# Kernel optimization log

Measured on AMD Instinct MI355X. Metric: run time of the kernel, lower is better.

Reference implementation:

```python
import jax, jax.numpy as jnp
import numpy as np

SEQ_LEN = 79
D_MODEL = 1024
BATCH = 512


def setup_inputs() -> dict:
    key = jax.random.key(0)
    ks = jax.random.split(key, 6)
    d = D_MODEL
    inp = {
        "x": jax.random.normal(ks[0], (BATCH, SEQ_LEN, d), dtype=jnp.float32),
        "piece_w": jax.random.normal(ks[1], (d, 6), dtype=jnp.float32) / np.sqrt(d),
        "piece_b": jnp.zeros((6,), dtype=jnp.float32),
        "color_w": jax.random.normal(ks[2], (d, 1), dtype=jnp.float32) / np.sqrt(d),
        "color_b": jnp.zeros((1,), dtype=jnp.float32),
        "mlp1_w": jax.random.normal(ks[3], (15, 32), dtype=jnp.float32) / np.sqrt(15.0),
        "mlp1_b": jnp.zeros((32,), dtype=jnp.float32),
        "mlp2_w": jax.random.normal(ks[4], (32, 8), dtype=jnp.float32) / np.sqrt(32.0),
        "mlp2_b": jnp.zeros((8,), dtype=jnp.float32),
    }
    return inp


def _spatial_feats(n, dtype):
    # dx, dy between board squares (idx < 64), zeros for non-board tokens
    idx = jnp.arange(n)
    is_board = idx < 64
    xc = jnp.where(is_board, idx // 8, 0)
    yc = jnp.where(is_board, idx % 8, 0)
    dx = xc[:, None] - xc[None, :]
    dy = yc[:, None] - yc[None, :]
    return jnp.stack([dx, dy], axis=-1).astype(dtype)  # (N, N, 2)


def reference(x, piece_w, piece_b, color_w, color_b, mlp1_w, mlp1_b, mlp2_w, mlp2_b):
    B, N, d = x.shape
    spatial = _spatial_feats(N, x.dtype)                      # (N, N, 2)
    piece_emb = jnp.einsum("bnd,de->bne", x, piece_w) + piece_b   # (B, N, 6)
    color_emb = jnp.einsum("bnd,de->bne", x, color_w) + color_b   # (B, N, 1)
    same_color = (color_emb[:, :, None, :] == color_emb[:, None, :, :]).astype(x.dtype)  # (B,N,N,1)
    pairwise = jnp.concatenate(
        [
            jnp.broadcast_to(spatial[None], (B, N, N, 2)),
            jnp.broadcast_to(piece_emb[:, :, None, :], (B, N, N, 6)),
            jnp.broadcast_to(piece_emb[:, None, :, :], (B, N, N, 6)),
            same_color,
        ],
        axis=-1,
    )  # (B, N, N, 15)
    h = jax.nn.gelu(pairwise @ mlp1_w + mlp1_b)               # (B, N, N, 32)
    bias = h @ mlp2_w + mlp2_b                                # (B, N, N, H)
    return jnp.transpose(bias, (0, 3, 1, 2))                  # (B, H, N, N)
```

## Files before the change

### kernel.cpp

```cpp
#include <hip/hip_runtime.h>

#define SEQ 79
#define DM 1024
#define BATCHN 512
#define NPB (SEQ * SEQ)
#define P 36
#define NWAVES 4

typedef float v2f   __attribute__((ext_vector_type(2)));
typedef float f32x4 __attribute__((ext_vector_type(4)));
typedef short short8 __attribute__((ext_vector_type(8)));

__device__ __forceinline__ unsigned cvt_pk_bf16(float lo, float hi) {
    unsigned r;
    asm("v_cvt_pk_bf16_f32 %0, %1, %2" : "=v"(r) : "v"(lo), "v"(hi));
    return r;
}

template <int CTRL>
__device__ __forceinline__ float dpp_add(float v) {
    int t = __builtin_amdgcn_update_dpp(0, __builtin_bit_cast(int, v),
                                        CTRL, 0xf, 0xf, false);
    return v + __builtin_bit_cast(float, t);
}

__device__ __forceinline__ v2f gelu2(v2f a) {
    const v2f C1 = {2.3022585093f, 2.3022585093f};
    const v2f C2 = {0.1029450750f, 0.1029450750f};
    v2f tt = a * (a * a * C2 + C1);
    v2f e;
    e.x = __builtin_amdgcn_exp2f(tt.x);
    e.y = __builtin_amdgcn_exp2f(tt.y);
    v2f ep = e + (v2f){1.f, 1.f};
    v2f r;
    r.x = __builtin_amdgcn_rcpf(ep.x);
    r.y = __builtin_amdgcn_rcpf(ep.y);
    return a - a * r;
}

__global__ __launch_bounds__(256, 2) void fused_bias(
    const float* __restrict__ x,
    const float* __restrict__ piece_w, const float* __restrict__ piece_b,
    const float* __restrict__ color_w, const float* __restrict__ color_b,
    const float* __restrict__ mlp1_w,  const float* __restrict__ mlp1_b,
    const float* __restrict__ mlp2_w,  const float* __restrict__ mlp2_b,
    float* __restrict__ out)
{
    __shared__ float uL[80 * P];
    __shared__ float vL[80 * P];
    __shared__ float colL[80];

    const int tid  = threadIdx.x;
    const int lane = tid & 63;
    const int wv   = tid >> 6;
    const int b    = blockIdx.x;
    const int k    = lane & 31;
    const bool is_u = (lane < 32);

    float wp[4][4][7];
#pragma unroll
    for (int q = 0; q < 4; ++q)
#pragma unroll
        for (int t = 0; t < 4; ++t) {
            const int c = q * 256 + lane * 4 + t;
#pragma unroll
            for (int e = 0; e < 6; ++e) wp[q][t][e] = piece_w[c * 6 + e];
            wp[q][t][6] = color_w[c];
        }

    float wsp0 = mlp1_w[0 * 32 + k];
    float wsp1 = mlp1_w[1 * 32 + k];
    if (!is_u) { wsp0 = -wsp0; wsp1 = -wsp1; }
    const float bias1 = is_u ? mlp1_b[k] : 0.0f;
    float wc[6];
#pragma unroll
    for (int c = 0; c < 6; ++c)
        wc[c] = mlp1_w[((is_u ? 2 : 8) + c) * 32 + k];
    float pb[6];
#pragma unroll
    for (int e = 0; e < 6; ++e) pb[e] = piece_b[e];
    const float cb = color_b[0];

    const int e16 = lane & 15;
    const int kq  = lane >> 4;
    const int k0  = kq * 8;

    union { unsigned w[4]; short8 s; } A;
#pragma unroll
    for (int w = 0; w < 4; ++w) {
        const float lo = (e16 < 8) ? mlp2_w[(k0 + 2 * w) * 8 + e16] : 0.0f;
        const float hi = (e16 < 8) ? mlp2_w[(k0 + 2 * w + 1) * 8 + e16] : 0.0f;
        A.w[w] = cvt_pk_bf16(lo, hi);
    }
    v2f w14p[4];
#pragma unroll
    for (int w = 0; w < 4; ++w)
        w14p[w] = (v2f){mlp1_w[14 * 32 + k0 + 2 * w], mlp1_w[14 * 32 + k0 + 2 * w + 1]};
    float b2v[4];
#pragma unroll
    for (int q = 0; q < 4; ++q)
        b2v[q] = (kq < 2) ? mlp2_b[kq * 4 + q] : 0.0f;

    if (wv == 0) {
        if (lane < P) vL[79 * P + lane] = 0.0f;
        if (lane == 0) colL[79] = 0.0f;
    }

    const float* xb = x + (size_t)b * SEQ * DM;
    for (int n = wv; n < SEQ; n += NWAVES) {
        const float4* xr = (const float4*)(xb + (size_t)n * DM);
        float4 xv[4];
#pragma unroll
        for (int q = 0; q < 4; ++q) xv[q] = xr[q * 64 + lane];

        float acc[7] = {0.f, 0.f, 0.f, 0.f, 0.f, 0.f, 0.f};
#pragma unroll
        for (int q = 0; q < 4; ++q) {
            const float xs[4] = {xv[q].x, xv[q].y, xv[q].z, xv[q].w};
#pragma unroll
            for (int t = 0; t < 4; ++t)
#pragma unroll
                for (int e = 0; e < 7; ++e)
                    acc[e] = fmaf(xs[t], wp[q][t][e], acc[e]);
        }

#pragma unroll
        for (int e = 0; e < 7; ++e) {
            acc[e] = dpp_add<0xB1>(acc[e]);
            acc[e] = dpp_add<0x4E>(acc[e]);
            acc[e] = dpp_add<0x124>(acc[e]);
            acc[e] = dpp_add<0x128>(acc[e]);
            acc[e] += __shfl_xor(acc[e], 16, 64);
            acc[e] += __shfl_xor(acc[e], 32, 64);
        }

        float p[6];
#pragma unroll
        for (int e = 0; e < 6; ++e) p[e] = acc[e] + pb[e];

        const float fx = (n < 64) ? (float)(n >> 3) : 0.0f;
        const float fy = (n < 64) ? (float)(n & 7) : 0.0f;

        float val = bias1;
        val = fmaf(fx, wsp0, val);
        val = fmaf(fy, wsp1, val);
#pragma unroll
        for (int c = 0; c < 6; ++c) val = fmaf(p[c], wc[c], val);

        float* dst = is_u ? uL : vL;
        dst[n * P + k] = val;
        if (lane == 0) colL[n] = acc[6] + cb;
    }

    __syncthreads();

    const size_t obb = (size_t)b * (8 * NPB);
    for (int i = wv; i < SEQ; i += NWAVES) {
        const float4 ua = *(const float4*)(uL + i * P + k0);
        const float4 ub = *(const float4*)(uL + i * P + k0 + 4);
        const float ci = colL[i];
        const float uu[8] = {ua.x, ua.y, ua.z, ua.w, ub.x, ub.y, ub.z, ub.w};

#pragma unroll
        for (int jt = 0; jt < 5; ++jt) {
            const int j = jt * 16 + e16;
            const float4 va = *(const float4*)(vL + j * P + k0);
            const float4 vb = *(const float4*)(vL + j * P + k0 + 4);
            const float sw = (ci == colL[j]) ? 1.0f : 0.0f;
            const v2f swp = {sw, sw};
            const float vv[8] = {va.x, va.y, va.z, va.w, vb.x, vb.y, vb.z, vb.w};

            union { unsigned w[4]; short8 s; } B;
#pragma unroll
            for (int w = 0; w < 4; ++w) {
                v2f a = {uu[2 * w] + vv[2 * w], uu[2 * w + 1] + vv[2 * w + 1]};
                a = a + swp * w14p[w];
                const v2f h = gelu2(a);
                B.w[w] = cvt_pk_bf16(h.x, h.y);
            }

            f32x4 acc2 = {0.f, 0.f, 0.f, 0.f};
            acc2 = __builtin_amdgcn_mfma_f32_16x16x32_bf16(A.s, B.s, acc2, 0, 0, 0);

            if (kq < 2 && j < SEQ) {
                float* o = out + obb + (size_t)(kq * 4) * NPB + (size_t)i * SEQ + j;
#pragma unroll
                for (int q = 0; q < 4; ++q)
                    o[(size_t)q * NPB] = acc2[q] + b2v[q];
            }
        }
    }
}

extern "C" void kernel_launch(void* const* d_in, const int* in_sizes, int n_in,
                              void* d_out, int out_size, void* d_ws, size_t ws_size,
                              hipStream_t stream) {
    const float* x       = (const float*)d_in[0];
    const float* piece_w = (const float*)d_in[1];
    const float* piece_b = (const float*)d_in[2];
    const float* color_w = (const float*)d_in[3];
    const float* color_b = (const float*)d_in[4];
    const float* mlp1_w  = (const float*)d_in[5];
    const float* mlp1_b  = (const float*)d_in[6];
    const float* mlp2_w  = (const float*)d_in[7];
    const float* mlp2_b  = (const float*)d_in[8];
    float* out = (float*)d_out;

    hipLaunchKernelGGL(fused_bias, dim3(BATCHN), dim3(256), 0, stream,
                       x, piece_w, piece_b, color_w, color_b,
                       mlp1_w, mlp1_b, mlp2_w, mlp2_b, out);
}
```

Before: 72.25 us.

## Split fused kernel into embedding and pairwise kernels via global workspace

```diff
diff --git a/kernel.cpp b/kernel.cpp
--- a/kernel.cpp
+++ b/kernel.cpp
@@ -3,9 +3,12 @@
 #define SEQ 79
 #define DM 1024
 #define BATCHN 512
+#define NROWS (BATCHN * SEQ)
 #define NPB (SEQ * SEQ)
 #define P 36
-#define NWAVES 4
+#define VOFF (SEQ * P)
+#define COFF (2 * SEQ * P)
+#define WS_PER_B 5776
 
 typedef float v2f   __attribute__((ext_vector_type(2)));
 typedef float f32x4 __attribute__((ext_vector_type(4)));
@@ -38,22 +41,16 @@
     return a - a * r;
 }
 
-__global__ __launch_bounds__(256, 2) void fused_bias(
+__global__ __launch_bounds__(256) void k1_embed(
     const float* __restrict__ x,
     const float* __restrict__ piece_w, const float* __restrict__ piece_b,
     const float* __restrict__ color_w, const float* __restrict__ color_b,
     const float* __restrict__ mlp1_w,  const float* __restrict__ mlp1_b,
-    const float* __restrict__ mlp2_w,  const float* __restrict__ mlp2_b,
-    float* __restrict__ out)
+    float* __restrict__ ws)
 {
-    __shared__ float uL[80 * P];
-    __shared__ float vL[80 * P];
-    __shared__ float colL[80];
-
-    const int tid  = threadIdx.x;
-    const int lane = tid & 63;
-    const int wv   = tid >> 6;
-    const int b    = blockIdx.x;
+    const int lane = threadIdx.x & 63;
+    const int wid  = (blockIdx.x * blockDim.x + threadIdx.x) >> 6;
+    const int nw   = (gridDim.x * blockDim.x) >> 6;
     const int k    = lane & 31;
     const bool is_u = (lane < 32);
 
@@ -81,34 +78,8 @@
     for (int e = 0; e < 6; ++e) pb[e] = piece_b[e];
     const float cb = color_b[0];
 
-    const int e16 = lane & 15;
-    const int kq  = lane >> 4;
-    const int k0  = kq * 8;
-
-    union { unsigned w[4]; short8 s; } A;
-#pragma unroll
-    for (int w = 0; w < 4; ++w) {
-        const float lo = (e16 < 8) ? mlp2_w[(k0 + 2 * w) * 8 + e16] : 0.0f;
-        const float hi = (e16 < 8) ? mlp2_w[(k0 + 2 * w + 1) * 8 + e16] : 0.0f;
-        A.w[w] = cvt_pk_bf16(lo, hi);
-    }
-    v2f w14p[4];
-#pragma unroll
-    for (int w = 0; w < 4; ++w)
-        w14p[w] = (v2f){mlp1_w[14 * 32 + k0 + 2 * w], mlp1_w[14 * 32 + k0 + 2 * w + 1]};
-    float b2v[4];
-#pragma unroll
-    for (int q = 0; q < 4; ++q)
-        b2v[q] = (kq < 2) ? mlp2_b[kq * 4 + q] : 0.0f;
-
-    if (wv == 0) {
-        if (lane < P) vL[79 * P + lane] = 0.0f;
-        if (lane == 0) colL[79] = 0.0f;
-    }
-
-    const float* xb = x + (size_t)b * SEQ * DM;
-    for (int n = wv; n < SEQ; n += NWAVES) {
-        const float4* xr = (const float4*)(xb + (size_t)n * DM);
+    for (int row = wid; row < NROWS; row += nw) {
+        const float4* xr = (const float4*)(x + (size_t)row * DM);
         float4 xv[4];
 #pragma unroll
         for (int q = 0; q < 4; ++q) xv[q] = xr[q * 64 + lane];
@@ -138,6 +109,8 @@
 #pragma unroll
         for (int e = 0; e < 6; ++e) p[e] = acc[e] + pb[e];
 
+        const int b = row / SEQ;
+        const int n = row - b * SEQ;
         const float fx = (n < 64) ? (float)(n >> 3) : 0.0f;
         const float fy = (n < 64) ? (float)(n & 7) : 0.0f;
 
@@ -147,47 +120,82 @@
 #pragma unroll
         for (int c = 0; c < 6; ++c) val = fmaf(p[c], wc[c], val);
 
-        float* dst = is_u ? uL : vL;
-        dst[n * P + k] = val;
-        if (lane == 0) colL[n] = acc[6] + cb;
+        ws[(size_t)b * WS_PER_B + (is_u ? 0 : VOFF) + n * P + k] = val;
+        if (lane == 0) ws[(size_t)b * WS_PER_B + COFF + n] = acc[6] + cb;
     }
-
-    __syncthreads();
-
+}
+
+__global__ __launch_bounds__(320) void k2_pair(
+    const float* __restrict__ ws,
+    const float* __restrict__ mlp1_w,
+    const float* __restrict__ mlp2_w, const float* __restrict__ mlp2_b,
+    float* __restrict__ out)
+{
+    const int lane = threadIdx.x & 63;
+    const int jt   = threadIdx.x >> 6;
+    const int blk  = blockIdx.x;
+    const int b    = blk >> 2;
+    const int iq   = blk & 3;
+
+    const int e16 = lane & 15;
+    const int kq  = lane >> 4;
+    const int k0  = kq * 8;
+
+    union { unsigned w[4]; short8 s; } A;
+#pragma unroll
+    for (int w = 0; w < 4; ++w) {
+        const float lo = (e16 < 8) ? mlp2_w[(k0 + 2 * w) * 8 + e16] : 0.0f;
+        const float hi = (e16 < 8) ? mlp2_w[(k0 + 2 * w + 1) * 8 + e16] : 0.0f;
+        A.w[w] = cvt_pk_bf16(lo, hi);
+    }
+    v2f w14p[4];
+#pragma unroll
+    for (int w = 0; w < 4; ++w)
+        w14p[w] = (v2f){mlp1_w[14 * 32 + k0 + 2 * w], mlp1_w[14 * 32 + k0 + 2 * w + 1]};
+    float b2v[4];
+#pragma unroll
+    for (int q = 0; q < 4; ++q)
+        b2v[q] = (kq < 2) ? mlp2_b[kq * 4 + q] : 0.0f;
+
+    const float* wsb = ws + (size_t)b * WS_PER_B;
+
+    const int j  = jt * 16 + e16;
+    const int jc = (j < SEQ) ? j : (SEQ - 1);
+    const float4 va = *(const float4*)(wsb + VOFF + jc * P + k0);
+    const float4 vb = *(const float4*)(wsb + VOFF + jc * P + k0 + 4);
+    const float vv[8] = {va.x, va.y, va.z, va.w, vb.x, vb.y, vb.z, vb.w};
+    const float cj = wsb[COFF + jc];
+
+    const int i0 = iq * 20;
+    const int i1 = (i0 + 20 < SEQ) ? i0 + 20 : SEQ;
     const size_t obb = (size_t)b * (8 * NPB);
-    for (int i = wv; i < SEQ; i += NWAVES) {
-        const float4 ua = *(const float4*)(uL + i * P + k0);
-        const float4 ub = *(const float4*)(uL + i * P + k0 + 4);
-        const float ci = colL[i];
+
+    for (int i = i0; i < i1; ++i) {
+        const float4 ua = *(const float4*)(wsb + i * P + k0);
+        const float4 ub = *(const float4*)(wsb + i * P + k0 + 4);
+        const float ci = wsb[COFF + i];
         const float uu[8] = {ua.x, ua.y, ua.z, ua.w, ub.x, ub.y, ub.z, ub.w};
 
-#pragma unroll
-        for (int jt = 0; jt < 5; ++jt) {
-            const int j = jt * 16 + e16;
-            const float4 va = *(const float4*)(vL + j * P + k0);
-            const float4 vb = *(const float4*)(vL + j * P + k0 + 4);
-            const float sw = (ci == colL[j]) ? 1.0f : 0.0f;
-            const v2f swp = {sw, sw};
-            const float vv[8] = {va.x, va.y, va.z, va.w, vb.x, vb.y, vb.z, vb.w};
-
-            union { unsigned w[4]; short8 s; } B;
-#pragma unroll
-            for (int w = 0; w < 4; ++w) {
-                v2f a = {uu[2 * w] + vv[2 * w], uu[2 * w + 1] + vv[2 * w + 1]};
-                a = a + swp * w14p[w];
-                const v2f h = gelu2(a);
-                B.w[w] = cvt_pk_bf16(h.x, h.y);
-            }
-
-            f32x4 acc2 = {0.f, 0.f, 0.f, 0.f};
-            acc2 = __builtin_amdgcn_mfma_f32_16x16x32_bf16(A.s, B.s, acc2, 0, 0, 0);
-
-            if (kq < 2 && j < SEQ) {
-                float* o = out + obb + (size_t)(kq * 4) * NPB + (size_t)i * SEQ + j;
-#pragma unroll
-                for (int q = 0; q < 4; ++q)
-                    o[(size_t)q * NPB] = acc2[q] + b2v[q];
-            }
+        const float sw = (ci == cj) ? 1.0f : 0.0f;
+        const v2f swp = {sw, sw};
+
+        union { unsigned w[4]; short8 s; } B;
+#pragma unroll
+        for (int w = 0; w < 4; ++w) {
+            v2f a = {uu[2 * w] + vv[2 * w], uu[2 * w + 1] + vv[2 * w + 1]};
+            a = a + swp * w14p[w];
+            const v2f h = gelu2(a);
+            B.w[w] = cvt_pk_bf16(h.x, h.y);
+        }
+
+        f32x4 acc2 = {0.f, 0.f, 0.f, 0.f};
+        acc2 = __builtin_amdgcn_mfma_f32_16x16x32_bf16(A.s, B.s, acc2, 0, 0, 0);
+
+        if (kq < 2 && j < SEQ) {
+            float* o = out + obb + (size_t)(kq * 4) * NPB + (size_t)i * SEQ + j;
+#pragma unroll
+            for (int q = 0; q < 4; ++q)
+                o[(size_t)q * NPB] = acc2[q] + b2v[q];
         }
     }
 }
@@ -205,8 +213,10 @@
     const float* mlp2_w  = (const float*)d_in[7];
     const float* mlp2_b  = (const float*)d_in[8];
     float* out = (float*)d_out;
-
-    hipLaunchKernelGGL(fused_bias, dim3(BATCHN), dim3(256), 0, stream,
-                       x, piece_w, piece_b, color_w, color_b,
-                       mlp1_w, mlp1_b, mlp2_w, mlp2_b, out);
-}
+    float* ws  = (float*)d_ws;
+
+    hipLaunchKernelGGL(k1_embed, dim3(2048), dim3(256), 0, stream,
+                       x, piece_w, piece_b, color_w, color_b, mlp1_w, mlp1_b, ws);
+    hipLaunchKernelGGL(k2_pair, dim3(BATCHN * 4), dim3(320), 0, stream,
+                       ws, mlp1_w, mlp2_w, mlp2_b, out);
+}
```

After: 85.10 us. 17.8% more time.
